# Kernel optimization log

Hardware: AMD Instinct MI355X
Metric: run time of the kernel (lower is better)

Reference implementation:

```python
import jax, jax.numpy as jnp
import numpy as np
from jax import lax

EPS = 1e-5

def prelu(x, a):
    # a: per-channel [C], x: [N,C,H,W]
    a = a[None, :, None, None]
    return jnp.where(x >= 0, x, a * x)

def batchnorm_train(x, gamma, beta):
    # training-mode BN: biased batch stats over (N,H,W)
    mean = jnp.mean(x, axis=(0, 2, 3), keepdims=True)
    var = jnp.mean((x - mean) ** 2, axis=(0, 2, 3), keepdims=True)
    xn = (x - mean) * lax.rsqrt(var + EPS)
    return xn * gamma[None, :, None, None] + beta[None, :, None, None]

def dw_conv3x3_sign(x, w):
    # binarize input and weights, depthwise 3x3 conv, padding=1
    C = x.shape[1]
    return lax.conv_general_dilated(
        jnp.sign(x), jnp.sign(w),
        window_strides=(1, 1), padding=((1, 1), (1, 1)),
        feature_group_count=C,
        dimension_numbers=('NCHW', 'OIHW', 'NCHW'))

def conv1x1_sign(x, w):
    # w: [O, C]; binarized 1x1 conv as einsum
    return jnp.einsum('nchw,oc->nohw', jnp.sign(x), jnp.sign(w))

def setup_inputs() -> dict:
    key = jax.random.key(0)
    ks = jax.random.split(key, 20)
    C_in, C_out = 256, 256
    x = jax.random.normal(ks[0], (32, C_in, 56, 56), dtype=jnp.float32)
    w_dw = jax.random.normal(ks[1], (C_in, 1, 3, 3), dtype=jnp.float32) * 0.1
    w1 = jax.random.normal(ks[2], (C_in, C_in), dtype=jnp.float32) * 0.05
    w2 = jax.random.normal(ks[3], (C_in, C_in), dtype=jnp.float32) * 0.05
    w3 = jax.random.normal(ks[4], (C_out, C_in), dtype=jnp.float32) * 0.05
    # PReLU init 0.25 (torch default), BN gamma=1 beta=0
    inp = {
        'x': x, 'w_dw': w_dw, 'w1': w1, 'w2': w2, 'w3': w3,
        'a1': jnp.full((C_in,), 0.25, jnp.float32),
        'a2': jnp.full((C_in,), 0.25, jnp.float32),
        'a3': jnp.full((C_in,), 0.25, jnp.float32),
        'a4': jnp.full((C_out,), 0.25, jnp.float32),
        'g1': jnp.ones((C_in,), jnp.float32), 'b1': jnp.zeros((C_in,), jnp.float32),
        'g2': jnp.ones((C_in,), jnp.float32), 'b2': jnp.zeros((C_in,), jnp.float32),
        'g3': jnp.ones((C_in,), jnp.float32), 'b3': jnp.zeros((C_in,), jnp.float32),
        'g4': jnp.ones((C_out,), jnp.float32), 'b4': jnp.zeros((C_out,), jnp.float32),
    }
    return inp

def reference(x, w_dw, w1, w2, w3, a1, a2, a3, a4, g1, b1, g2, b2, g3, b3, g4, b4):
    residual1 = x
    # out = x.sign(); BinaryConv2d signs its input again (idempotent)
    out = dw_conv3x3_sign(jnp.sign(x), w_dw)
    out = batchnorm_train(prelu(out, a1), g1, b1)
    out = out + residual1
    residual2 = out
    out = conv1x1_sign(jnp.sign(out), w1)
    out = batchnorm_train(prelu(out, a2), g2, b2)
    out = out + residual2
    out = conv1x1_sign(jnp.sign(out), w2)
    out = batchnorm_train(prelu(out, a3), g3, b3)
    out = conv1x1_sign(jnp.sign(out), w3)
    out = batchnorm_train(prelu(out, a4), g4, b4)
    return out
```

## Files before the change

kernel.cpp:

```cpp
#include <hip/hip_runtime.h>
#include <stdint.h>
#include <stddef.h>
#include <math.h>

#define HWSZ   3136
#define NPIX   100352

typedef __attribute__((ext_vector_type(4))) float f32x4;
typedef __attribute__((ext_vector_type(8))) short bf16x8;
typedef __attribute__((ext_vector_type(8))) unsigned short u16x8;

__device__ __forceinline__ float bf2f(unsigned short u) {
  union { float f; unsigned int i; } v; v.i = ((unsigned int)u) << 16; return v.f;
}
__device__ __forceinline__ unsigned short f2bf(float f) {
  union { float f; unsigned int i; } v; v.f = f;
  return (unsigned short)((v.i + 0x7FFFu + ((v.i >> 16) & 1u)) >> 16);
}
__device__ __forceinline__ unsigned short sgnf_bf16(float v) {
  return (v > 0.f) ? 0x3F80u : ((v < 0.f) ? 0xBF80u : 0u);
}
__device__ __forceinline__ int isgn(float v) {
  return (v > 0.f) ? 1 : ((v < 0.f) ? -1 : 0);
}

__global__ __launch_bounds__(256) void k_prepw(const float* __restrict__ w1,
    const float* __restrict__ w2, const float* __restrict__ w3,
    unsigned short* __restrict__ bs)
{
  int idx = blockIdx.x * 256 + threadIdx.x;
  int wsel = idx >> 16, rem = idx & 65535;
  const float* wp = (wsel == 0) ? w1 : ((wsel == 1) ? w2 : w3);
  float v = wp[rem];
  bs[idx] = sgnf_bf16(v);
}

__global__ __launch_bounds__(256) void k_dwconv(const float* __restrict__ x,
    const float* __restrict__ wdw, const float* __restrict__ a1,
    signed char* __restrict__ c1, float* __restrict__ P1)
{
  __shared__ float sp[58 * 60];
  __shared__ float rs[4];
  int bid = blockIdx.x;
  int c = bid & 255;
  int t = threadIdx.x;
  const float* xp = x + (size_t)bid * HWSZ;

  for (int i = t; i < 58 * 60; i += 256) sp[i] = 0.f;
  __syncthreads();
  for (int q = t; q < 784; q += 256) {
    int h = q / 14, w0 = (q - h * 14) * 4;
    f32x4 v = *(const f32x4*)(xp + h * 56 + w0);
    float* d = sp + (h + 1) * 60 + (w0 + 2);
    d[0] = (float)isgn(v[0]);
    d[1] = (float)isgn(v[1]);
    d[2] = (float)isgn(v[2]);
    d[3] = (float)isgn(v[3]);
  }
  float wsf[9];
  #pragma unroll
  for (int i = 0; i < 9; i++) wsf[i] = (float)isgn(wdw[c * 9 + i]);
  float av = a1[c];
  __syncthreads();

  float lsum = 0.f;
  signed char* outp = c1 + (size_t)bid * HWSZ;
  for (int q = t; q < 784; q += 256) {
    int h = q / 14, w0 = (q - h * 14) * 4;
    float win[3][8];
    #pragma unroll
    for (int r = 0; r < 3; r++) {
      const float* rowp = sp + (h + r) * 60 + w0;
      *(f32x4*)(&win[r][0]) = *(const f32x4*)rowp;
      *(f32x4*)(&win[r][4]) = *(const f32x4*)(rowp + 4);
    }
    unsigned int pk = 0;
    #pragma unroll
    for (int j = 0; j < 4; j++) {
      float acc = 0.f;
      #pragma unroll
      for (int r = 0; r < 3; r++) {
        acc = fmaf(win[r][j + 1], wsf[r * 3 + 0], acc);
        acc = fmaf(win[r][j + 2], wsf[r * 3 + 1], acc);
        acc = fmaf(win[r][j + 3], wsf[r * 3 + 2], acc);
      }
      int ia = (int)acc;
      pk |= ((unsigned int)(unsigned char)(signed char)ia) << (8 * j);
      lsum += (acc >= 0.f) ? acc : av * acc;
    }
    *(unsigned int*)(void*)(outp + h * 56 + w0) = pk;
  }
  for (int o = 32; o > 0; o >>= 1) lsum += __shfl_xor(lsum, o);
  if ((t & 63) == 0) rs[t >> 6] = lsum;
  __syncthreads();
  if (t == 0) P1[bid] = ((rs[0] + rs[1]) + (rs[2] + rs[3]));
}

__global__ __launch_bounds__(256) void k_cmb(const float* __restrict__ P,
    float* __restrict__ M)
{
  int c = threadIdx.x;
  float acc = 0.f;
  for (int n = 0; n < 32; n++) acc = __fadd_rn(acc, P[n * 256 + c]);
  M[c] = __fdiv_rn(acc, 100352.0f);
}

__global__ __launch_bounds__(256) void k_cmbG(const float* __restrict__ PM,
    float* __restrict__ M)
{
  int c = threadIdx.x;
  float acc = 0.f;
  for (int b = 0; b < 784; b++) acc = __fadd_rn(acc, PM[(size_t)b * 256 + c]);
  M[c] = __fdiv_rn(acc, 100352.0f);
}


__global__ __launch_bounds__(256) void k_var1(const signed char* __restrict__ c1,
    const float* __restrict__ a1, const float* __restrict__ M,
    float* __restrict__ PV)
{
  __shared__ float rr[256];
  __shared__ float lsm[32];
  int bid = blockIdx.x;
  int c = bid & 255;
  int t = threadIdx.x;
  int lf = t >> 3, j = t & 7;
  const int base = (lf >> 2) * 392 + (lf & 3) * 96;
  const int nb = ((lf & 3) == 3) ? 13 : 12;
  const signed char* pl = c1 + (size_t)bid * HWSZ + base + j;
  float av = a1[c], m = M[c];
  float r;
  {
    float v = (float)(int)pl[0];
    float tt = (v >= 0.f) ? v : __fmul_rn(av, v);
    float d = __fsub_rn(tt, m);
    r = __fmul_rn(d, d);
  }
  for (int b = 1; b < nb; b++) {
    float v = (float)(int)pl[8 * b];
    float tt = (v >= 0.f) ? v : __fmul_rn(av, v);
    float d = __fsub_rn(tt, m);
    r = __fadd_rn(r, __fmul_rn(d, d));
  }
  rr[t] = r;
  __syncthreads();
  if (j == 0) {
    const float* q = rr + lf * 8;
    lsm[lf] = __fadd_rn(
        __fadd_rn(__fadd_rn(q[0], q[1]), __fadd_rn(q[2], q[3])),
        __fadd_rn(__fadd_rn(q[4], q[5]), __fadd_rn(q[6], q[7])));
  }
  __syncthreads();
  if (t == 0) {
    float ch[8];
    #pragma unroll
    for (int q8 = 0; q8 < 8; q8++)
      ch[q8] = __fadd_rn(__fadd_rn(lsm[q8 * 4], lsm[q8 * 4 + 1]),
                         __fadd_rn(lsm[q8 * 4 + 2], lsm[q8 * 4 + 3]));
    float s0 = __fadd_rn(ch[0], ch[1]), s1 = __fadd_rn(ch[2], ch[3]);
    float s2 = __fadd_rn(ch[4], ch[5]), s3 = __fadd_rn(ch[6], ch[7]);
    PV[bid] = __fadd_rn(__fadd_rn(s0, s1), __fadd_rn(s2, s3));
  }
}

__global__ __launch_bounds__(256) void k_vcmb(const float* __restrict__ PV,
    float* __restrict__ R)
{
  int c = threadIdx.x;
  float acc = 0.f;
  for (int n = 0; n < 32; n++) acc = __fadd_rn(acc, PV[n * 256 + c]);
  float v = __fdiv_rn(acc, 100352.0f);
  R[c] = (float)(1.0 / sqrt((double)__fadd_rn(v, 1e-5f)));
}

__global__ __launch_bounds__(256) void k_varT(const unsigned short* __restrict__ tb,
    const float* __restrict__ M, float* __restrict__ PVL)
{
  int n = blockIdx.x >> 5, lf = blockIdx.x & 31;
  int c = threadIdx.x;
  const int base = (lf >> 2) * 392 + (lf & 3) * 96;
  const int nb = ((lf & 3) == 3) ? 13 : 12;
  const unsigned short* pl = tb + ((size_t)n * HWSZ + base) * 256 + c;
  float m = M[c];
  float r[8];
  #pragma unroll
  for (int j = 0; j < 8; j++) {
    float d = __fsub_rn(bf2f(pl[(size_t)j * 256]), m);
    r[j] = __fmul_rn(d, d);
  }
  for (int b = 1; b < nb; b++) {
    #pragma unroll
    for (int j = 0; j < 8; j++) {
      float d = __fsub_rn(bf2f(pl[(size_t)(8 * b + j) * 256]), m);
      r[j] = __fadd_rn(r[j], __fmul_rn(d, d));
    }
  }
  float lv = __fadd_rn(
      __fadd_rn(__fadd_rn(r[0], r[1]), __fadd_rn(r[2], r[3])),
      __fadd_rn(__fadd_rn(r[4], r[5]), __fadd_rn(r[6], r[7])));
  PVL[(size_t)blockIdx.x * 256 + c] = lv;
}

__global__ __launch_bounds__(256) void k_vcmbT(const float* __restrict__ PVL,
    float* __restrict__ R)
{
  int c = threadIdx.x;
  float acc = 0.f;
  for (int n = 0; n < 32; n++) {
    float ch[8];
    #pragma unroll
    for (int q = 0; q < 8; q++) {
      const float* p = PVL + ((size_t)(n * 32 + q * 4)) * 256 + c;
      ch[q] = __fadd_rn(__fadd_rn(p[0], p[256]), __fadd_rn(p[512], p[768]));
    }
    float s0 = __fadd_rn(ch[0], ch[1]), s1 = __fadd_rn(ch[2], ch[3]);
    float s2 = __fadd_rn(ch[4], ch[5]), s3 = __fadd_rn(ch[6], ch[7]);
    float plane = __fadd_rn(__fadd_rn(s0, s1), __fadd_rn(s2, s3));
    acc = __fadd_rn(acc, plane);
  }
  float v = __fdiv_rn(acc, 100352.0f);
  R[c] = (float)(1.0 / sqrt((double)__fadd_rn(v, 1e-5f)));
}

__global__ __launch_bounds__(256) void k_apply1(const float* __restrict__ x,
    const signed char* __restrict__ c1, const float* __restrict__ a1,
    const float* __restrict__ M1, const float* __restrict__ R1,
    const float* __restrict__ g1, const float* __restrict__ b1,
    unsigned short* __restrict__ s1)
{
  __shared__ __align__(16) unsigned short lb[32 * 264];
  int bid = blockIdx.x;
  int n = bid / 98, pb = bid % 98;
  int px0 = pb * 32;
  int t = threadIdx.x;

  int pxg = (t & 7) * 4, cb = t >> 3;
  #pragma unroll
  for (int j = 0; j < 8; j++) {
    int c = cb + j * 32;
    size_t gidx = ((size_t)(n * 256 + c)) * HWSZ + px0 + pxg;
    f32x4 xv = *(const f32x4*)(x + gidx);
    unsigned int cp = *(const unsigned int*)(const void*)(c1 + gidx);
    float av = a1[c];
    float m1 = M1[c], r1 = R1[c], gg1 = g1[c], bb1 = b1[c];
    #pragma unroll
    for (int e = 0; e < 4; e++) {
      int row = pxg + e;
      int idx = row * 264 + (c ^ (((row >> 2) & 7) << 3));
      float v = (float)(int)(signed char)(unsigned char)(cp >> (8 * e));
      float t1 = (v >= 0.f) ? v : __fmul_rn(av, v);
      float xn = __fmul_rn(__fsub_rn(t1, m1), r1);
      float bn = __fadd_rn(__fmul_rn(xn, gg1), bb1);
      float o1 = __fadd_rn(bn, xv[e]);
      lb[idx] = sgnf_bf16(o1);
    }
  }
  __syncthreads();
  unsigned short* sp = s1 + ((size_t)(n * HWSZ + px0)) * 256;
  for (int j = 0; j < 4; j++) {
    int f = j * 256 + t;
    int px = f >> 5, c16 = f & 31;
    int cs = (c16 ^ ((px >> 2) & 7)) * 8;
    *(u16x8*)(sp + px * 256 + c16 * 8) = *(const u16x8*)(lb + px * 264 + cs);
  }
}

__global__ __launch_bounds__(256) void k_apply2(const float* __restrict__ x,
    const signed char* __restrict__ c1, const unsigned short* __restrict__ t2,
    const float* __restrict__ a1,
    const float* __restrict__ M1, const float* __restrict__ R1,
    const float* __restrict__ g1, const float* __restrict__ b1,
    const float* __restrict__ M2, const float* __restrict__ R2,
    const float* __restrict__ g2, const float* __restrict__ b2,
    unsigned short* __restrict__ s2)
{
  __shared__ __align__(16) unsigned short lb[32 * 264];
  int bid = blockIdx.x;
  int n = bid / 98, pb = bid % 98;
  int px0 = pb * 32;
  int t = threadIdx.x;

  const unsigned short* tp = t2 + ((size_t)(n * HWSZ + px0)) * 256;
  for (int j = 0; j < 4; j++) {
    int f = j * 256 + t;
    int px = f >> 5, c16 = f & 31;
    int cs = (c16 ^ ((px >> 2) & 7)) * 8;
    *(u16x8*)(lb + px * 264 + cs) = *(const u16x8*)(tp + px * 256 + c16 * 8);
  }
  __syncthreads();

  int pxg = (t & 7) * 4, cb = t >> 3;
  #pragma unroll
  for (int j = 0; j < 8; j++) {
    int c = cb + j * 32;
    size_t gidx = ((size_t)(n * 256 + c)) * HWSZ + px0 + pxg;
    f32x4 xv = *(const f32x4*)(x + gidx);
    unsigned int cp = *(const unsigned int*)(const void*)(c1 + gidx);
    float av = a1[c];
    float m1 = M1[c], r1 = R1[c], gg1 = g1[c], bb1 = b1[c];
    float m2 = M2[c], r2 = R2[c], gg2 = g2[c], bb2 = b2[c];
    #pragma unroll
    for (int e = 0; e < 4; e++) {
      int row = pxg + e;
      int idx = row * 264 + (c ^ (((row >> 2) & 7) << 3));
      float v = (float)(int)(signed char)(unsigned char)(cp >> (8 * e));
      float t1 = (v >= 0.f) ? v : __fmul_rn(av, v);
      float xn1 = __fmul_rn(__fsub_rn(t1, m1), r1);
      float bn1v = __fadd_rn(__fmul_rn(xn1, gg1), bb1);
      float o1 = __fadd_rn(bn1v, xv[e]);
      float t2v = bf2f(lb[idx]);
      float xn2 = __fmul_rn(__fsub_rn(t2v, m2), r2);
      float bn2v = __fadd_rn(__fmul_rn(xn2, gg2), bb2);
      float o2 = __fadd_rn(bn2v, o1);
      lb[idx] = sgnf_bf16(o2);
    }
  }
  __syncthreads();
  unsigned short* sp = s2 + ((size_t)(n * HWSZ + px0)) * 256;
  for (int j = 0; j < 4; j++) {
    int f = j * 256 + t;
    int px = f >> 5, c16 = f & 31;
    int cs = (c16 ^ ((px >> 2) & 7)) * 8;
    *(u16x8*)(sp + px * 256 + c16 * 8) = *(const u16x8*)(lb + px * 264 + cs);
  }
}

__global__ __launch_bounds__(256) void k_apply3(const unsigned short* __restrict__ t3,
    const float* __restrict__ M3, const float* __restrict__ R3,
    const float* __restrict__ g3, const float* __restrict__ b3,
    unsigned short* __restrict__ s3)
{
  size_t idx = ((size_t)blockIdx.x * 256 + threadIdx.x) * 8;
  int c0 = (int)(idx & 255);
  u16x8 v = *(const u16x8*)(t3 + idx);
  u16x8 o;
  #pragma unroll
  for (int e = 0; e < 8; e++) {
    int c = c0 + e;
    float t = bf2f(v[e]);
    float xn = __fmul_rn(__fsub_rn(t, M3[c]), R3[c]);
    float bn = __fadd_rn(__fmul_rn(xn, g3[c]), b3[c]);
    o[e] = sgnf_bf16(bn);
  }
  *(u16x8*)(s3 + idx) = o;
}

__global__ __launch_bounds__(256) void k_final(const unsigned short* __restrict__ t4,
    const float* __restrict__ M4, const float* __restrict__ R4,
    const float* __restrict__ g4, const float* __restrict__ b4,
    float* __restrict__ outp)
{
  __shared__ __align__(16) float lt[16 * 260];
  int bid = blockIdx.x;
  int n = bid / 196, pb = bid % 196;
  int px0 = pb * 16;
  int t = threadIdx.x;

  const unsigned short* tp = t4 + ((size_t)(n * HWSZ + px0)) * 256;
  for (int j = 0; j < 2; j++) {
    int f = j * 256 + t;
    int px = f >> 5, c16 = f & 31;
    u16x8 v = *(const u16x8*)(tp + px * 256 + c16 * 8);
    f32x4 o0, o1;
    #pragma unroll
    for (int e = 0; e < 4; e++) {
      int c = c16 * 8 + e;
      float tv = bf2f(v[e]);
      float xn = __fmul_rn(__fsub_rn(tv, M4[c]), R4[c]);
      o0[e] = __fadd_rn(__fmul_rn(xn, g4[c]), b4[c]);
    }
    #pragma unroll
    for (int e = 0; e < 4; e++) {
      int c = c16 * 8 + 4 + e;
      float tv = bf2f(v[4 + e]);
      float xn = __fmul_rn(__fsub_rn(tv, M4[c]), R4[c]);
      o1[e] = __fadd_rn(__fmul_rn(xn, g4[c]), b4[c]);
    }
    *(f32x4*)(lt + px * 260 + c16 * 8) = o0;
    *(f32x4*)(lt + px * 260 + c16 * 8 + 4) = o1;
  }
  __syncthreads();
  for (int j = 0; j < 4; j++) {
    int f = j * 256 + t;
    int c = f >> 2, q = f & 3;
    f32x4 v;
    #pragma unroll
    for (int e = 0; e < 4; e++) v[e] = lt[(q * 4 + e) * 260 + c];
    *(f32x4*)(outp + ((size_t)(n * 256 + c)) * HWSZ + px0 + q * 4) = v;
  }
}

__global__ __launch_bounds__(512) void k_gemm(
    const unsigned short* __restrict__ sIn, const unsigned short* __restrict__ bsg,
    const float* __restrict__ aP, unsigned short* __restrict__ tOut,
    float* __restrict__ PM)
{
  __shared__ __align__(16) unsigned short As[128 * 72];
  __shared__ __align__(16) unsigned short Bs[256 * 72];
  __shared__ float red[8][4][16];
  const int t = threadIdx.x;
  const int lane = t & 63;
  const int wid = t >> 6;
  const int wm = wid >> 2, wn = wid & 3;
  const int lr = lane & 15, lk = lane >> 4;
  const int pix0 = blockIdx.x * 128;
  const unsigned short* Ap = sIn + (size_t)pix0 * 256;

  f32x4 acc[4][4];
  #pragma unroll
  for (int i = 0; i < 4; i++)
    #pragma unroll
    for (int j = 0; j < 4; j++)
      acc[i][j] = (f32x4){0.f, 0.f, 0.f, 0.f};

  for (int kt = 0; kt < 4; kt++) {
    const int k0 = kt * 64;
    if (kt) __syncthreads();
    #pragma unroll
    for (int j = 0; j < 2; j++) {
      int idx = j * 512 + t;
      int row = idx >> 3, kc = idx & 7;
      u16x8 v = *(const u16x8*)(Ap + (size_t)row * 256 + k0 + kc * 8);
      *(u16x8*)(As + row * 72 + kc * 8) = v;
    }
    #pragma unroll
    for (int j = 0; j < 4; j++) {
      int idx = j * 512 + t;
      int row = idx >> 3, kc = idx & 7;
      u16x8 v = *(const u16x8*)(bsg + (size_t)row * 256 + k0 + kc * 8);
      *(u16x8*)(Bs + row * 72 + kc * 8) = v;
    }
    __syncthreads();
    #pragma unroll
    for (int h = 0; h < 2; h++) {
      bf16x8 af[4], bfr[4];
      #pragma unroll
      for (int mf = 0; mf < 4; mf++)
        af[mf] = *(const bf16x8*)(As + (wm * 64 + mf * 16 + lr) * 72 + (h * 4 + lk) * 8);
      #pragma unroll
      for (int nf = 0; nf < 4; nf++)
        bfr[nf] = *(const bf16x8*)(Bs + (wn * 64 + nf * 16 + lr) * 72 + (h * 4 + lk) * 8);
      #pragma unroll
      for (int mf = 0; mf < 4; mf++)
        #pragma unroll
        for (int nf = 0; nf < 4; nf++)
          acc[mf][nf] = __builtin_amdgcn_mfma_f32_16x16x32_bf16(
              af[mf], bfr[nf], acc[mf][nf], 0, 0, 0);
    }
  }

  float csum[4];
  #pragma unroll
  for (int nf = 0; nf < 4; nf++) csum[nf] = 0.f;

  #pragma unroll
  for (int nf = 0; nf < 4; nf++) {
    int gcol = wn * 64 + nf * 16 + lr;
    float av = aP[gcol];
    #pragma unroll
    for (int mf = 0; mf < 4; mf++) {
      #pragma unroll
      for (int r = 0; r < 4; r++) {
        int grow = pix0 + wm * 64 + mf * 16 + lk * 4 + r;
        float u = acc[mf][nf][r];
        float tv = (u >= 0.f) ? u : __fmul_rn(av, u);
        tOut[(size_t)grow * 256 + gcol] = f2bf(tv);
        csum[nf] = __fadd_rn(csum[nf], tv);
      }
    }
  }
  #pragma unroll
  for (int nf = 0; nf < 4; nf++) {
    csum[nf] = __fadd_rn(csum[nf], __shfl_xor(csum[nf], 16));
    csum[nf] = __fadd_rn(csum[nf], __shfl_xor(csum[nf], 32));
  }
  if (lane < 16) {
    #pragma unroll
    for (int nf = 0; nf < 4; nf++) red[wid][nf][lane] = csum[nf];
  }
  __syncthreads();
  if (t < 256) {
    int wn2 = t >> 6, nf2 = (t >> 4) & 3, lr2 = t & 15;
    PM[(size_t)blockIdx.x * 256 + t] =
        __fadd_rn(red[wn2][nf2][lr2], red[wn2 + 4][nf2][lr2]);
  }
}

extern "C" void kernel_launch(void* const* d_in, const int* in_sizes, int n_in,
                              void* d_out, int out_size, void* d_ws, size_t ws_size,
                              hipStream_t stream)
{
  const float* x   = (const float*)d_in[0];
  const float* wdw = (const float*)d_in[1];
  const float* w1  = (const float*)d_in[2];
  const float* w2  = (const float*)d_in[3];
  const float* w3  = (const float*)d_in[4];
  const float* a1  = (const float*)d_in[5];
  const float* a2  = (const float*)d_in[6];
  const float* a3  = (const float*)d_in[7];
  const float* a4  = (const float*)d_in[8];
  const float* g1  = (const float*)d_in[9];
  const float* b1  = (const float*)d_in[10];
  const float* g2  = (const float*)d_in[11];
  const float* b2  = (const float*)d_in[12];
  const float* g3  = (const float*)d_in[13];
  const float* b3  = (const float*)d_in[14];
  const float* g4  = (const float*)d_in[15];
  const float* b4  = (const float*)d_in[16];

  char* ws = (char*)d_ws;
  unsigned short* SB  = (unsigned short*)ws;
  unsigned short* TB  = (unsigned short*)(ws + 51380224);
  signed char*    c1  = (signed char*)(ws + 102760448);
  unsigned short* BS  = (unsigned short*)(ws + 128450560);
  float*          BIG = (float*)(ws + 128843776);
  float*          PV  = (float*)(ws + 129892352);
  float*          MR  = (float*)(ws + 129925120);
  float*          outp = (float*)d_out;

  float* P1  = BIG;
  float* PM  = BIG;
  float* PVL = BIG;
  float* M1 = MR;        float* R1 = MR + 256;
  float* M2 = MR + 512;  float* R2 = MR + 768;
  float* M3 = MR + 1024; float* R3 = MR + 1280;
  float* M4 = MR + 1536; float* R4 = MR + 1792;

  k_prepw <<<dim3(768),  dim3(256), 0, stream>>>(w1, w2, w3, BS);
  k_dwconv<<<dim3(8192), dim3(256), 0, stream>>>(x, wdw, a1, c1, P1);

  k_cmb   <<<dim3(1),    dim3(256), 0, stream>>>(P1, M1);
  k_var1  <<<dim3(8192), dim3(256), 0, stream>>>(c1, a1, M1, PV);
  k_vcmb  <<<dim3(1),    dim3(256), 0, stream>>>(PV, R1);
  k_apply1<<<dim3(3136), dim3(256), 0, stream>>>(x, c1, a1, M1, R1, g1, b1, SB);

  k_gemm  <<<dim3(784),  dim3(512), 0, stream>>>(SB, BS, a2, TB, PM);
  k_cmbG  <<<dim3(1),    dim3(256), 0, stream>>>(PM, M2);
  k_varT  <<<dim3(1024), dim3(256), 0, stream>>>(TB, M2, PVL);
  k_vcmbT <<<dim3(1),    dim3(256), 0, stream>>>(PVL, R2);
  k_apply2<<<dim3(3136), dim3(256), 0, stream>>>(x, c1, TB, a1,
                                                 M1, R1, g1, b1, M2, R2, g2, b2, SB);

  k_gemm  <<<dim3(784),  dim3(512), 0, stream>>>(SB, BS + 65536, a3, TB, PM);
  k_cmbG  <<<dim3(1),    dim3(256), 0, stream>>>(PM, M3);
  k_varT  <<<dim3(1024), dim3(256), 0, stream>>>(TB, M3, PVL);
  k_vcmbT <<<dim3(1),    dim3(256), 0, stream>>>(PVL, R3);
  k_apply3<<<dim3(12544),dim3(256), 0, stream>>>(TB, M3, R3, g3, b3, SB);

  k_gemm  <<<dim3(784),  dim3(512), 0, stream>>>(SB, BS + 131072, a4, TB, PM);
  k_cmbG  <<<dim3(1),    dim3(256), 0, stream>>>(PM, M4);
  k_varT  <<<dim3(1024), dim3(256), 0, stream>>>(TB, M4, PVL);
  k_vcmbT <<<dim3(1),    dim3(256), 0, stream>>>(PVL, R4);
  k_final <<<dim3(6272), dim3(256), 0, stream>>>(TB, M4, R4, g4, b4, outp);
}
```

Measured before the change: 509.5 us.

## Swizzle GEMM LDS tiles and stage epilogue through shared memory

Replaces the padded LDS layout for the A and B tiles with an XOR-swizzled 64-wide layout, which shrinks shared memory use while avoiding bank conflicts. The epilogue now writes PReLU outputs as bf16 into a shared staging buffer, one half of the rows at a time, and then stores them to global memory as coalesced 16-byte rows instead of scattered 2-byte stores. Per-channel partial sums are now computed from the rounded bf16 values read back from LDS, which slightly changes the summation numerics. Launch bounds request higher occupancy, at the cost of extra barriers in the epilogue.

```diff
diff --git a/kernel.cpp b/kernel.cpp
--- a/kernel.cpp
+++ b/kernel.cpp
@@ -390,14 +390,16 @@
   }
 }
 
-__global__ __launch_bounds__(512) void k_gemm(
+__global__ __launch_bounds__(512, 6) void k_gemm(
     const unsigned short* __restrict__ sIn, const unsigned short* __restrict__ bsg,
     const float* __restrict__ aP, unsigned short* __restrict__ tOut,
     float* __restrict__ PM)
 {
-  __shared__ __align__(16) unsigned short As[128 * 72];
-  __shared__ __align__(16) unsigned short Bs[256 * 72];
-  __shared__ float red[8][4][16];
+  __shared__ __align__(16) char smem[49152];
+  unsigned short* As = (unsigned short*)smem;
+  unsigned short* Bs = (unsigned short*)(smem + 16384);
+  unsigned short* Cs = (unsigned short*)smem;
+  float* red = (float*)(smem + 33792);
   const int t = threadIdx.x;
   const int lane = t & 63;
   const int wid = t >> 6;
@@ -421,25 +423,31 @@
       int idx = j * 512 + t;
       int row = idx >> 3, kc = idx & 7;
       u16x8 v = *(const u16x8*)(Ap + (size_t)row * 256 + k0 + kc * 8);
-      *(u16x8*)(As + row * 72 + kc * 8) = v;
+      *(u16x8*)(As + row * 64 + ((kc ^ (row & 7)) * 8)) = v;
     }
     #pragma unroll
     for (int j = 0; j < 4; j++) {
       int idx = j * 512 + t;
       int row = idx >> 3, kc = idx & 7;
       u16x8 v = *(const u16x8*)(bsg + (size_t)row * 256 + k0 + kc * 8);
-      *(u16x8*)(Bs + row * 72 + kc * 8) = v;
+      *(u16x8*)(Bs + row * 64 + ((kc ^ (row & 7)) * 8)) = v;
     }
     __syncthreads();
     #pragma unroll
     for (int h = 0; h < 2; h++) {
       bf16x8 af[4], bfr[4];
       #pragma unroll
-      for (int mf = 0; mf < 4; mf++)
-        af[mf] = *(const bf16x8*)(As + (wm * 64 + mf * 16 + lr) * 72 + (h * 4 + lk) * 8);
+      for (int mf = 0; mf < 4; mf++) {
+        int row = wm * 64 + mf * 16 + lr;
+        int ch = (h * 4 + lk) ^ (row & 7);
+        af[mf] = *(const bf16x8*)(As + row * 64 + ch * 8);
+      }
       #pragma unroll
-      for (int nf = 0; nf < 4; nf++)
-        bfr[nf] = *(const bf16x8*)(Bs + (wn * 64 + nf * 16 + lr) * 72 + (h * 4 + lk) * 8);
+      for (int nf = 0; nf < 4; nf++) {
+        int nrow = wn * 64 + nf * 16 + lr;
+        int ch = (h * 4 + lk) ^ (nrow & 7);
+        bfr[nf] = *(const bf16x8*)(Bs + nrow * 64 + ch * 8);
+      }
       #pragma unroll
       for (int mf = 0; mf < 4; mf++)
         #pragma unroll
@@ -449,40 +457,57 @@
     }
   }
 
-  float csum[4];
-  #pragma unroll
-  for (int nf = 0; nf < 4; nf++) csum[nf] = 0.f;
-
-  #pragma unroll
-  for (int nf = 0; nf < 4; nf++) {
-    int gcol = wn * 64 + nf * 16 + lr;
-    float av = aP[gcol];
-    #pragma unroll
-    for (int mf = 0; mf < 4; mf++) {
+  float lsum[8];
+  #pragma unroll
+  for (int e = 0; e < 8; e++) lsum[e] = 0.f;
+
+  #pragma unroll
+  for (int h = 0; h < 2; h++) {
+    __syncthreads();
+    if (wm == h) {
       #pragma unroll
-      for (int r = 0; r < 4; r++) {
-        int grow = pix0 + wm * 64 + mf * 16 + lk * 4 + r;
-        float u = acc[mf][nf][r];
-        float tv = (u >= 0.f) ? u : __fmul_rn(av, u);
-        tOut[(size_t)grow * 256 + gcol] = f2bf(tv);
-        csum[nf] = __fadd_rn(csum[nf], tv);
+      for (int nf = 0; nf < 4; nf++) {
+        int col = wn * 64 + nf * 16 + lr;
+        float av = aP[col];
+        #pragma unroll
+        for (int mf = 0; mf < 4; mf++) {
+          #pragma unroll
+          for (int r = 0; r < 4; r++) {
+            int row = mf * 16 + lk * 4 + r;
+            float u = acc[mf][nf][r];
+            float tv = (u >= 0.f) ? u : __fmul_rn(av, u);
+            Cs[row * 264 + col] = f2bf(tv);
+          }
+        }
       }
     }
-  }
-  #pragma unroll
-  for (int nf = 0; nf < 4; nf++) {
-    csum[nf] = __fadd_rn(csum[nf], __shfl_xor(csum[nf], 16));
-    csum[nf] = __fadd_rn(csum[nf], __shfl_xor(csum[nf], 32));
-  }
-  if (lane < 16) {
-    #pragma unroll
-    for (int nf = 0; nf < 4; nf++) red[wid][nf][lane] = csum[nf];
+    __syncthreads();
+    #pragma unroll
+    for (int j = 0; j < 4; j++) {
+      int f = j * 512 + t;
+      int row = f >> 5, c16 = f & 31;
+      u16x8 v = *(const u16x8*)(Cs + row * 264 + c16 * 8);
+      *(u16x8*)(tOut + ((size_t)(pix0 + h * 64 + row)) * 256 + c16 * 8) = v;
+      #pragma unroll
+      for (int e = 0; e < 8; e++)
+        lsum[e] = __fadd_rn(lsum[e], bf2f(v[e]));
+    }
+  }
+  #pragma unroll
+  for (int e = 0; e < 8; e++)
+    lsum[e] = __fadd_rn(lsum[e], __shfl_xor(lsum[e], 32));
+  if (lane < 32) {
+    #pragma unroll
+    for (int e = 0; e < 8; e++) red[(wid * 32 + lane) * 8 + e] = lsum[e];
   }
   __syncthreads();
   if (t < 256) {
-    int wn2 = t >> 6, nf2 = (t >> 4) & 3, lr2 = t & 15;
-    PM[(size_t)blockIdx.x * 256 + t] =
-        __fadd_rn(red[wn2][nf2][lr2], red[wn2 + 4][nf2][lr2]);
+    int c16 = t >> 3, e = t & 7;
+    float S = 0.f;
+    #pragma unroll
+    for (int w = 0; w < 8; w++)
+      S = __fadd_rn(S, red[((w * 32 + c16) * 8 + e)]);
+    PM[(size_t)blockIdx.x * 256 + t] = S;
   }
 }
 
```

After: 772.2 us. 1.52x slower.
